# Kernel tuning notes

Measured on AMD Instinct MI355X. Metric: run time of the kernel, lower is better.

## Reference

```python
import jax, jax.numpy as jnp
import numpy as np

NUM_VECTORS = 8192
LATENT_DIM = 256
BETA = 0.25


def setup_inputs() -> dict:
    key = jax.random.key(0)
    k1, k2 = jax.random.split(key)
    z = jax.random.normal(k1, (16, LATENT_DIM, 32, 32), dtype=jnp.float32)
    # nn.Embedding weight initialized uniform(-1/K, 1/K)
    emb_weight = jax.random.uniform(
        k2, (NUM_VECTORS, LATENT_DIM), dtype=jnp.float32,
        minval=-1.0 / NUM_VECTORS, maxval=1.0 / NUM_VECTORS)
    return {"z": z, "emb_weight": emb_weight}


def reference(z, emb_weight):
    # z: [B, C, H, W] -> [B, H, W, C]
    z_bhwc = jnp.transpose(z, (0, 2, 3, 1))
    B, H, W, C = z_bhwc.shape
    z_flat = z_bhwc.reshape(-1, C)  # [N, C]

    # Squared distances: ||z||^2 + ||e||^2 - 2 z.e  -> [N, K]
    d = (jnp.sum(z_flat ** 2, axis=1, keepdims=True)
         + jnp.sum(emb_weight ** 2, axis=1)
         - 2.0 * jnp.einsum('nc,kc->nk', z_flat, emb_weight))
    idx = jnp.argmin(d, axis=1)  # [N]

    z_q = emb_weight[idx].reshape(B, H, W, C)

    sg = jax.lax.stop_gradient
    loss = (jnp.mean((sg(z_q) - z_bhwc) ** 2)
            + BETA * jnp.mean((z_q - sg(z_bhwc)) ** 2))

    # Straight-through estimator
    z_q_st = z_bhwc + sg(z_q - z_bhwc)
    z_q_out = jnp.transpose(z_q_st, (0, 3, 1, 2))  # [B, C, H, W]
    return z_q_out, idx, loss
```

## Files before the change

### kernel.cpp

```cpp
#include <hip/hip_runtime.h>
#include <math.h>

#define NB   16
#define CC   256
#define NPTS 16384
#define KK   8192
#define Z_OUT 4194304

#define WS_ENORM 16448
#define LCAP     96
#define MARGIN   4.0e-4f

typedef short v8s __attribute__((ext_vector_type(8)));
typedef float v4f __attribute__((ext_vector_type(4)));

__device__ __forceinline__ void gl_lds16(const void* g, void* l) {
    __builtin_amdgcn_global_load_lds((const __attribute__((address_space(1))) void*)g,
                                     (__attribute__((address_space(3))) void*)l, 16, 0, 0);
}
__device__ __forceinline__ unsigned short f2bf(float f) {
    unsigned int u = __float_as_uint(f);
    return (unsigned short)((u + 0x7FFFu + ((u >> 16) & 1u)) >> 16);
}
__device__ __forceinline__ unsigned fenc(float f) {
    unsigned u = __float_as_uint(f);
    return (u & 0x80000000u) ? ~u : (u | 0x80000000u);
}
__device__ __forceinline__ float fdec(unsigned m) {
    unsigned u = (m & 0x80000000u) ? (m & 0x7fffffffu) : ~m;
    return __uint_as_float(u);
}

__global__ void k_prep(const float* __restrict__ z, const float* __restrict__ emb,
                       unsigned short* __restrict__ zb16, unsigned short* __restrict__ ebf,
                       float* __restrict__ enorm, float* __restrict__ lossAcc,
                       int* __restrict__ doneCnt) {
    const int bid = blockIdx.x;
    const int tid = threadIdx.x;
    if (bid < 2048) {
        const int w = tid >> 6, lane = tid & 63;
        const int k = bid * 4 + w;
        const int i = k * CC + lane * 4;
        float4 v = *(const float4*)(emb + i);
        *(ushort4*)(ebf + i) = make_ushort4(f2bf(v.x), f2bf(v.y), f2bf(v.z), f2bf(v.w));
        float s = v.x * v.x + v.y * v.y + v.z * v.z + v.w * v.w;
        for (int off = 32; off > 0; off >>= 1) s += __shfl_down(s, off);
        if (lane == 0) enorm[k] = s;
        if (bid == 0 && tid == 0) { lossAcc[0] = 0.0f; doneCnt[0] = 0; }
    } else {
        __shared__ float ts[64][65];
        const int b2 = bid - 2048;
        const int hw0 = (b2 & 15) * 64, c0 = ((b2 >> 4) & 3) * 64, b = b2 >> 6;
#pragma unroll
        for (int p = 0; p < 4; ++p) {
            int u = p * 256 + tid;
            int ci = u >> 4, j4 = (u & 15) << 2;
            float4 v = *(const float4*)(z + (size_t)b * 262144 + (size_t)(c0 + ci) * 1024 + hw0 + j4);
            ts[ci][j4 + 0] = v.x; ts[ci][j4 + 1] = v.y; ts[ci][j4 + 2] = v.z; ts[ci][j4 + 3] = v.w;
        }
        __syncthreads();
#pragma unroll
        for (int p = 0; p < 4; ++p) {
            int u = p * 256 + tid;
            int hj = u >> 4, i4 = (u & 15) << 2;
            ushort4 o = make_ushort4(f2bf(ts[i4 + 0][hj]), f2bf(ts[i4 + 1][hj]),
                                     f2bf(ts[i4 + 2][hj]), f2bf(ts[i4 + 3][hj]));
            *(ushort4*)(zb16 + (size_t)(b * 1024 + hw0 + hj) * 256 + c0 + i4) = o;
        }
    }
}

__global__ __launch_bounds__(512, 2)
void k_cand(const unsigned short* __restrict__ zb16, const unsigned short* __restrict__ ebf,
            const float* __restrict__ z, const float* __restrict__ emb,
            const float* __restrict__ enorm, float* __restrict__ idxf) {
    __shared__ short    Bs[8][4][512];
    __shared__ unsigned runmaxU[64];
    __shared__ int      cnt[64];
    __shared__ int      lstK[64][LCAP];
    __shared__ float    lstD[64][LCAP];
    __shared__ float    zl[64][257];

    const int tid  = threadIdx.x;
    const int lane = tid & 63;
    const int w    = tid >> 6;
    const int nb   = blockIdx.x << 6;
    const int m16  = lane & 15, q = lane >> 4;

    if (tid < 64) { runmaxU[tid] = 0x007FFFFFu;  cnt[tid] = 0; }

#pragma unroll
    for (int p = 0; p < 4; ++p) {
        const int g8 = p * 8 + w;
        const int cc = g8 >> 2, nt = g8 & 3;
        const unsigned short* g = zb16 + (size_t)(nb + nt * 16 + m16) * 256 + cc * 32 + q * 8;
        gl_lds16(g, &Bs[cc][nt][lane * 8]);
    }

    auto loadA = [&](v8s (&a)[4], int kbr, int cc) {
#pragma unroll
        for (int kt = 0; kt < 4; ++kt)
            a[kt] = *(const v8s*)(ebf + (size_t)(kbr + (kt << 4) + m16) * 256 + (cc << 5) + q * 8);
    };
    auto loadB = [&](v8s (&b)[4], int cc) {
#pragma unroll
        for (int nt = 0; nt < 4; ++nt) b[nt] = *(const v8s*)&Bs[cc][nt][lane * 8];
    };

    v8s aR[4][4];
    v8s bP[4], bN[4];

    const int kb0 = w << 6;
    loadA(aR[0], kb0, 0);
    loadA(aR[1], kb0, 1);
    loadA(aR[2], kb0, 2);
    __syncthreads();
    loadB(bP, 0);

#pragma unroll 1
    for (int s = 0; s < 16; ++s) {
        const int kb  = ((s << 3) + w) << 6;
        const int kbn = (s < 15) ? kb + 512 : kb;
        v4f acc[16];
#pragma unroll
        for (int i = 0; i < 16; ++i) acc[i] = (v4f){0.f, 0.f, 0.f, 0.f};

#pragma unroll
        for (int cc = 0; cc < 8; ++cc) {
            if ((cc & 1) == 0) loadB(bN, (cc + 1) & 7);
            else               loadB(bP, (cc + 1) & 7);
            {
                const int tcc = cc + 3;
                if (tcc < 8) loadA(aR[tcc & 3], kb,  tcc);
                else         loadA(aR[tcc & 3], kbn, tcc - 8);
            }
#pragma unroll
            for (int kt = 0; kt < 4; ++kt)
#pragma unroll
                for (int nt = 0; nt < 4; ++nt)
                    acc[kt * 4 + nt] = __builtin_amdgcn_mfma_f32_16x16x32_bf16(
                        aR[cc & 3][kt], ((cc & 1) ? bN[nt] : bP[nt]),
                        acc[kt * 4 + nt], 0, 0, 0);
        }

        float mx[4];
#pragma unroll
        for (int nt = 0; nt < 4; ++nt) {
            float m = acc[0 * 4 + nt][0];
#pragma unroll
            for (int kt = 0; kt < 4; ++kt)
#pragma unroll
                for (int r = 0; r < 4; ++r) m = fmaxf(m, acc[kt * 4 + nt][r]);
            m = fmaxf(m, __shfl_xor(m, 16));
            m = fmaxf(m, __shfl_xor(m, 32));
            mx[nt] = m;
            if (lane < 16) atomicMax(&runmaxU[nt * 16 + lane], fenc(m));
        }
#pragma unroll
        for (int nt = 0; nt < 4; ++nt) {
            const int nl = nt * 16 + m16;
            const float thr = fmaxf(fdec(runmaxU[nl]), mx[nt]) - MARGIN;
#pragma unroll
            for (int kt = 0; kt < 4; ++kt)
#pragma unroll
                for (int r = 0; r < 4; ++r) {
                    if (acc[kt * 4 + nt][r] >= thr) {
                        int k = kb + (kt << 4) + q * 4 + r;
                        int pos = atomicAdd(&cnt[nl], 1);
                        if (pos < LCAP) { lstK[nl][pos] = k; lstD[nl][pos] = acc[kt * 4 + nt][r]; }
                    }
                }
        }
        if (s == 3 || s == 9) __syncthreads();
    }

    __syncthreads();

    {
        const int b = nb >> 10, hw0 = nb & 1023;
#pragma unroll
        for (int p = 0; p < 8; ++p) {
            const int u = p * 512 + tid;
            const int c = u >> 4, j4 = (u & 15) << 2;
            float4 v = *(const float4*)(z + (size_t)b * 262144 + (size_t)c * 1024 + hw0 + j4);
            zl[j4 + 0][c] = v.x; zl[j4 + 1][c] = v.y; zl[j4 + 2][c] = v.z; zl[j4 + 3][c] = v.w;
        }
    }
    __syncthreads();

#pragma unroll 1
    for (int rr = 0; rr < 8; ++rr) {
        const int nl = w * 8 + rr;
        const int n  = nb + nl;
        const float4 zv = *(const float4*)&zl[nl][lane * 4];
        float zn = zv.x * zv.x;
        zn = fmaf(zv.y, zv.y, zn); zn = fmaf(zv.z, zv.z, zn); zn = fmaf(zv.w, zv.w, zn);
#pragma unroll
        for (int off = 1; off < 64; off <<= 1) zn += __shfl_xor(zn, off);
        const int cl = cnt[nl];
        float bd = __builtin_inff();
        int   bk = 0x7fffffff;
        if (cl <= 64) {
            int  ki = 0;
            bool pass = false;
            if (lane < cl) {
                ki = lstK[nl][lane];
                pass = (lstD[nl][lane] >= fdec(runmaxU[nl]) - MARGIN);
            }
            unsigned long long mask = __ballot(pass);
            int kc = -1;
            float4 ev;
            if (mask) {
                const int j0 = __ffsll(mask) - 1; mask &= mask - 1;
                kc = __shfl(ki, j0);
                ev = *(const float4*)(emb + (size_t)kc * CC + lane * 4);
            }
            while (kc >= 0) {
                const int    kcur = kc;
                const float4 evc  = ev;
                if (mask) {
                    const int jn = __ffsll(mask) - 1; mask &= mask - 1;
                    kc = __shfl(ki, jn);
                    ev = *(const float4*)(emb + (size_t)kc * CC + lane * 4);
                } else kc = -1;
                float p = zv.x * evc.x;
                p = fmaf(zv.y, evc.y, p);
                p = fmaf(zv.z, evc.z, p);
                p = fmaf(zv.w, evc.w, p);
#pragma unroll
                for (int off = 1; off < 64; off <<= 1) p += __shfl_xor(p, off);
                const float d = (zn + enorm[kcur]) - (p + p);
                if (d < bd || (d == bd && kcur < bk)) { bd = d; bk = kcur; }
            }
        } else {
#pragma unroll 1
            for (int k = 0; k < KK; ++k) {
                const float4 ev = *(const float4*)(emb + (size_t)k * CC + lane * 4);
                float p = zv.x * ev.x;
                p = fmaf(zv.y, ev.y, p);
                p = fmaf(zv.z, ev.z, p);
                p = fmaf(zv.w, ev.w, p);
#pragma unroll
                for (int off = 1; off < 64; off <<= 1) p += __shfl_xor(p, off);
                const float d = (zn + enorm[k]) - (p + p);
                if (d < bd) { bd = d; bk = k; }
            }
        }
        if (lane == 0) idxf[n] = (float)bk;
    }
}

__global__ __launch_bounds__(256)
void k_gather(const float* __restrict__ z, const float* __restrict__ emb,
              const float* __restrict__ idxf, float* __restrict__ out,
              float* __restrict__ lossAcc, int* __restrict__ doneCnt,
              float* __restrict__ outLoss) {
    __shared__ float red[256];
    const int bid = blockIdx.x;
    const int b = bid >> 5, h = bid & 31;
    const int t = threadIdx.x;
    const int w_ = t & 31, cg = t >> 5;
    const int n = b * 1024 + h * 32 + w_;
    const int ki = (int)idxf[n];
    const float* ep = emb + (size_t)ki * CC;
    const size_t base = (size_t)b * 262144 + h * 32 + w_;
    float ls = 0.0f;
#pragma unroll 4
    for (int c = cg; c < CC; c += 8) {
        float e = ep[c];
        size_t a = base + (size_t)c * 1024;
        float zv = z[a];
        out[a] = e;
        float df = e - zv;
        ls = fmaf(df, df, ls);
    }
    red[t] = ls;
    __syncthreads();
    for (int s = 128; s > 0; s >>= 1) {
        if (t < s) red[t] += red[t + s];
        __syncthreads();
    }
    if (t == 0) {
        atomicAdd(lossAcc, red[0]);
        __threadfence();
        int old = atomicAdd(doneCnt, 1);
        if (old == (int)gridDim.x - 1) {
            float tot = atomicAdd(lossAcc, 0.0f);
            float m = tot * (1.0f / 4194304.0f);
            outLoss[0] = m + 0.25f * m;
        }
    }
}

extern "C" void kernel_launch(void* const* d_in, const int* in_sizes, int n_in,
                              void* d_out, int out_size, void* d_ws, size_t ws_size,
                              hipStream_t stream) {
    const float* z   = (const float*)d_in[0];
    const float* emb = (const float*)d_in[1];
    float* outf = (float*)d_out;
    float* wsf  = (float*)d_ws;

    float* lossAcc = wsf;
    int*   doneCnt = (int*)(wsf + 1);
    float* enorm   = wsf + WS_ENORM;

    unsigned short* zb16 = (unsigned short*)outf;
    unsigned short* ebf  = (unsigned short*)(outf + 2097152);

    k_prep<<<3072, 256, 0, stream>>>(z, emb, zb16, ebf, enorm, lossAcc, doneCnt);
    k_cand<<<256, 512, 0, stream>>>(zb16, ebf, z, emb, enorm, outf + Z_OUT);
    k_gather<<<512, 256, 0, stream>>>(z, emb, outf + Z_OUT, outf,
                                      lossAcc, doneCnt, outf + Z_OUT + NPTS);
}
```

Baseline: 255.3 us.

## Fuse z transpose/bf16 conversion and gather/loss into candidate kernel

Removes the separate z transpose-to-bf16 pass and the gather/loss kernel. k_cand now loads its z tile into LDS up front, builds the bf16 B fragments from it directly, and after picking indices writes the chosen embedding rows back into the same LDS tile. That tile is then stored transposed to the output, with the loss accumulated per block. This saves two global round trips of z-sized data and one kernel launch. In exchange it adds LDS conversion work before the MFMA loop and output stores at the end of k_cand.

```diff
diff --git a/kernel.cpp b/kernel.cpp
--- a/kernel.cpp
+++ b/kernel.cpp
@@ -8,16 +8,13 @@
 #define Z_OUT 4194304
 
 #define WS_ENORM 16448
+#define WS_EBF   32768
 #define LCAP     96
 #define MARGIN   4.0e-4f
 
 typedef short v8s __attribute__((ext_vector_type(8)));
 typedef float v4f __attribute__((ext_vector_type(4)));
 
-__device__ __forceinline__ void gl_lds16(const void* g, void* l) {
-    __builtin_amdgcn_global_load_lds((const __attribute__((address_space(1))) void*)g,
-                                     (__attribute__((address_space(3))) void*)l, 16, 0, 0);
-}
 __device__ __forceinline__ unsigned short f2bf(float f) {
     unsigned int u = __float_as_uint(f);
     return (unsigned short)((u + 0x7FFFu + ((u >> 16) & 1u)) >> 16);
@@ -31,70 +28,62 @@
     return __uint_as_float(u);
 }
 
-__global__ void k_prep(const float* __restrict__ z, const float* __restrict__ emb,
-                       unsigned short* __restrict__ zb16, unsigned short* __restrict__ ebf,
+__global__ void k_prep(const float* __restrict__ emb, unsigned short* __restrict__ ebf,
                        float* __restrict__ enorm, float* __restrict__ lossAcc,
                        int* __restrict__ doneCnt) {
-    const int bid = blockIdx.x;
-    const int tid = threadIdx.x;
-    if (bid < 2048) {
-        const int w = tid >> 6, lane = tid & 63;
-        const int k = bid * 4 + w;
-        const int i = k * CC + lane * 4;
-        float4 v = *(const float4*)(emb + i);
-        *(ushort4*)(ebf + i) = make_ushort4(f2bf(v.x), f2bf(v.y), f2bf(v.z), f2bf(v.w));
-        float s = v.x * v.x + v.y * v.y + v.z * v.z + v.w * v.w;
-        for (int off = 32; off > 0; off >>= 1) s += __shfl_down(s, off);
-        if (lane == 0) enorm[k] = s;
-        if (bid == 0 && tid == 0) { lossAcc[0] = 0.0f; doneCnt[0] = 0; }
-    } else {
-        __shared__ float ts[64][65];
-        const int b2 = bid - 2048;
-        const int hw0 = (b2 & 15) * 64, c0 = ((b2 >> 4) & 3) * 64, b = b2 >> 6;
-#pragma unroll
-        for (int p = 0; p < 4; ++p) {
-            int u = p * 256 + tid;
-            int ci = u >> 4, j4 = (u & 15) << 2;
-            float4 v = *(const float4*)(z + (size_t)b * 262144 + (size_t)(c0 + ci) * 1024 + hw0 + j4);
-            ts[ci][j4 + 0] = v.x; ts[ci][j4 + 1] = v.y; ts[ci][j4 + 2] = v.z; ts[ci][j4 + 3] = v.w;
-        }
-        __syncthreads();
-#pragma unroll
-        for (int p = 0; p < 4; ++p) {
-            int u = p * 256 + tid;
-            int hj = u >> 4, i4 = (u & 15) << 2;
-            ushort4 o = make_ushort4(f2bf(ts[i4 + 0][hj]), f2bf(ts[i4 + 1][hj]),
-                                     f2bf(ts[i4 + 2][hj]), f2bf(ts[i4 + 3][hj]));
-            *(ushort4*)(zb16 + (size_t)(b * 1024 + hw0 + hj) * 256 + c0 + i4) = o;
-        }
-    }
+    const int w = threadIdx.x >> 6, lane = threadIdx.x & 63;
+    const int k = blockIdx.x * 4 + w;
+    const int i = k * CC + lane * 4;
+    float4 v = *(const float4*)(emb + i);
+    *(ushort4*)(ebf + i) = make_ushort4(f2bf(v.x), f2bf(v.y), f2bf(v.z), f2bf(v.w));
+    float s = v.x * v.x + v.y * v.y + v.z * v.z + v.w * v.w;
+    for (int off = 32; off > 0; off >>= 1) s += __shfl_down(s, off);
+    if (lane == 0) enorm[k] = s;
+    if (blockIdx.x == 0 && threadIdx.x == 0) { lossAcc[0] = 0.0f; doneCnt[0] = 0; }
 }
 
 __global__ __launch_bounds__(512, 2)
-void k_cand(const unsigned short* __restrict__ zb16, const unsigned short* __restrict__ ebf,
-            const float* __restrict__ z, const float* __restrict__ emb,
-            const float* __restrict__ enorm, float* __restrict__ idxf) {
+void k_cand(const unsigned short* __restrict__ ebf, const float* __restrict__ z,
+            const float* __restrict__ emb, const float* __restrict__ enorm,
+            float* __restrict__ out, float* __restrict__ idxf,
+            float* __restrict__ lossAcc, int* __restrict__ doneCnt,
+            float* __restrict__ outLoss) {
     __shared__ short    Bs[8][4][512];
     __shared__ unsigned runmaxU[64];
     __shared__ int      cnt[64];
     __shared__ int      lstK[64][LCAP];
     __shared__ float    lstD[64][LCAP];
     __shared__ float    zl[64][257];
+    __shared__ float    lossP[8];
 
     const int tid  = threadIdx.x;
     const int lane = tid & 63;
     const int w    = tid >> 6;
     const int nb   = blockIdx.x << 6;
+    const int b    = nb >> 10, hw0 = nb & 1023;
     const int m16  = lane & 15, q = lane >> 4;
 
     if (tid < 64) { runmaxU[tid] = 0x007FFFFFu;  cnt[tid] = 0; }
+
+#pragma unroll
+    for (int p = 0; p < 8; ++p) {
+        const int u = p * 512 + tid;
+        const int c = u >> 4, j4 = (u & 15) << 2;
+        float4 v = *(const float4*)(z + (size_t)b * 262144 + (size_t)c * 1024 + hw0 + j4);
+        zl[j4 + 0][c] = v.x; zl[j4 + 1][c] = v.y; zl[j4 + 2][c] = v.z; zl[j4 + 3][c] = v.w;
+    }
+    __syncthreads();
 
 #pragma unroll
     for (int p = 0; p < 4; ++p) {
         const int g8 = p * 8 + w;
         const int cc = g8 >> 2, nt = g8 & 3;
-        const unsigned short* g = zb16 + (size_t)(nb + nt * 16 + m16) * 256 + cc * 32 + q * 8;
-        gl_lds16(g, &Bs[cc][nt][lane * 8]);
+        const int row = nt * 16 + m16, col = cc * 32 + q * 8;
+        float4 va = *(const float4*)&zl[row][col];
+        float4 vb = *(const float4*)&zl[row][col + 4];
+        ushort4* dst = (ushort4*)&Bs[cc][nt][lane * 8];
+        dst[0] = make_ushort4(f2bf(va.x), f2bf(va.y), f2bf(va.z), f2bf(va.w));
+        dst[1] = make_ushort4(f2bf(vb.x), f2bf(vb.y), f2bf(vb.z), f2bf(vb.w));
     }
 
     auto loadA = [&](v8s (&a)[4], int kbr, int cc) {
@@ -102,9 +91,9 @@
         for (int kt = 0; kt < 4; ++kt)
             a[kt] = *(const v8s*)(ebf + (size_t)(kbr + (kt << 4) + m16) * 256 + (cc << 5) + q * 8);
     };
-    auto loadB = [&](v8s (&b)[4], int cc) {
-#pragma unroll
-        for (int nt = 0; nt < 4; ++nt) b[nt] = *(const v8s*)&Bs[cc][nt][lane * 8];
+    auto loadB = [&](v8s (&bfrag)[4], int cc) {
+#pragma unroll
+        for (int nt = 0; nt < 4; ++nt) bfrag[nt] = *(const v8s*)&Bs[cc][nt][lane * 8];
     };
 
     v8s aR[4][4];
@@ -176,18 +165,7 @@
 
     __syncthreads();
 
-    {
-        const int b = nb >> 10, hw0 = nb & 1023;
-#pragma unroll
-        for (int p = 0; p < 8; ++p) {
-            const int u = p * 512 + tid;
-            const int c = u >> 4, j4 = (u & 15) << 2;
-            float4 v = *(const float4*)(z + (size_t)b * 262144 + (size_t)c * 1024 + hw0 + j4);
-            zl[j4 + 0][c] = v.x; zl[j4 + 1][c] = v.y; zl[j4 + 2][c] = v.z; zl[j4 + 3][c] = v.w;
-        }
-    }
-    __syncthreads();
-
+    float wls = 0.0f;
 #pragma unroll 1
     for (int rr = 0; rr < 8; ++rr) {
         const int nl = w * 8 + rr;
@@ -247,41 +225,32 @@
             }
         }
         if (lane == 0) idxf[n] = (float)bk;
-    }
-}
-
-__global__ __launch_bounds__(256)
-void k_gather(const float* __restrict__ z, const float* __restrict__ emb,
-              const float* __restrict__ idxf, float* __restrict__ out,
-              float* __restrict__ lossAcc, int* __restrict__ doneCnt,
-              float* __restrict__ outLoss) {
-    __shared__ float red[256];
-    const int bid = blockIdx.x;
-    const int b = bid >> 5, h = bid & 31;
-    const int t = threadIdx.x;
-    const int w_ = t & 31, cg = t >> 5;
-    const int n = b * 1024 + h * 32 + w_;
-    const int ki = (int)idxf[n];
-    const float* ep = emb + (size_t)ki * CC;
-    const size_t base = (size_t)b * 262144 + h * 32 + w_;
-    float ls = 0.0f;
-#pragma unroll 4
-    for (int c = cg; c < CC; c += 8) {
-        float e = ep[c];
-        size_t a = base + (size_t)c * 1024;
-        float zv = z[a];
-        out[a] = e;
-        float df = e - zv;
-        ls = fmaf(df, df, ls);
-    }
-    red[t] = ls;
-    __syncthreads();
-    for (int s = 128; s > 0; s >>= 1) {
-        if (t < s) red[t] += red[t + s];
-        __syncthreads();
-    }
-    if (t == 0) {
-        atomicAdd(lossAcc, red[0]);
+        const float4 ew = *(const float4*)(emb + (size_t)bk * CC + lane * 4);
+        float dx = ew.x - zv.x, dy = ew.y - zv.y, dz2 = ew.z - zv.z, dw = ew.w - zv.w;
+        float ls = dx * dx;
+        ls = fmaf(dy, dy, ls); ls = fmaf(dz2, dz2, ls); ls = fmaf(dw, dw, ls);
+#pragma unroll
+        for (int off = 1; off < 64; off <<= 1) ls += __shfl_xor(ls, off);
+        wls += ls;
+        zl[nl][lane * 4 + 0] = ew.x; zl[nl][lane * 4 + 1] = ew.y;
+        zl[nl][lane * 4 + 2] = ew.z; zl[nl][lane * 4 + 3] = ew.w;
+    }
+    if (lane == 0) lossP[w] = wls;
+    __syncthreads();
+
+#pragma unroll
+    for (int p = 0; p < 8; ++p) {
+        const int u = p * 512 + tid;
+        const int c = u >> 4, j4 = (u & 15) << 2;
+        float4 o = make_float4(zl[j4 + 0][c], zl[j4 + 1][c], zl[j4 + 2][c], zl[j4 + 3][c]);
+        *(float4*)(out + (size_t)b * 262144 + (size_t)c * 1024 + hw0 + j4) = o;
+    }
+
+    if (tid == 0) {
+        float bl = lossP[0];
+#pragma unroll
+        for (int i = 1; i < 8; ++i) bl += lossP[i];
+        atomicAdd(lossAcc, bl);
         __threadfence();
         int old = atomicAdd(doneCnt, 1);
         if (old == (int)gridDim.x - 1) {
@@ -303,12 +272,10 @@
     float* lossAcc = wsf;
     int*   doneCnt = (int*)(wsf + 1);
     float* enorm   = wsf + WS_ENORM;
-
-    unsigned short* zb16 = (unsigned short*)outf;
-    unsigned short* ebf  = (unsigned short*)(outf + 2097152);
-
-    k_prep<<<3072, 256, 0, stream>>>(z, emb, zb16, ebf, enorm, lossAcc, doneCnt);
-    k_cand<<<256, 512, 0, stream>>>(zb16, ebf, z, emb, enorm, outf + Z_OUT);
-    k_gather<<<512, 256, 0, stream>>>(z, emb, outf + Z_OUT, outf,
-                                      lossAcc, doneCnt, outf + Z_OUT + NPTS);
-}
+    unsigned short* ebf = (unsigned short*)(wsf + WS_EBF);
+
+    k_prep<<<2048, 256, 0, stream>>>(emb, ebf, enorm, lossAcc, doneCnt);
+    k_cand<<<256, 512, 0, stream>>>(ebf, z, emb, enorm,
+                                    outf, outf + Z_OUT, lossAcc, doneCnt,
+                                    outf + Z_OUT + NPTS);
+}
```

After: 237.1 us. 7.1% less time.
